# Kernel optimization log

Hardware: AMD Instinct MI355X
Metric: run time of the kernel (lower is better)

The kernel has to match this reference:

```python
import jax, jax.numpy as jnp
import numpy as np

B, S, D, H, R = 8, 1024, 1024, 8, 32
DH = D // H  # 128


def setup_inputs() -> dict:
    key = jax.random.key(0)
    ks = jax.random.split(key, 10)
    p = lambda k, shape: jax.random.normal(k, shape, dtype=jnp.float32) * 0.02
    return {
        "x": jax.random.normal(ks[0], (B, S, D), dtype=jnp.float32),
        "Uq": p(ks[1], (H, DH, R)), "Vq": p(ks[2], (H, R, DH)), "bq": p(ks[3], (H, DH)),
        "Uk": p(ks[4], (H, DH, R)), "Vk": p(ks[5], (H, R, DH)), "bk": p(ks[6], (H, DH)),
        "Uv": p(ks[7], (H, DH, R)), "Vv": p(ks[8], (H, R, DH)), "bv": p(ks[9], (H, DH)),
    }


def _lowrank(xh, U, V, b):
    # xh: [B,S,H,DH]; per-head factored linear y = x @ V^T @ U^T + b
    t = jnp.einsum('bshd,hrd->bshr', xh, V)          # down-project to rank R
    return jnp.einsum('bshr,hdr->bshd', t, U) + b    # up-project back to DH


def reference(x, Uq, Vq, bq, Uk, Vk, bk, Uv, Vv, bv):
    b_, s_, _ = x.shape
    xh = x.reshape(b_, s_, H, DH)                    # split heads (matches head-slice loop)
    q = _lowrank(xh, Uq, Vq, bq)
    k = _lowrank(xh, Uk, Vk, bk)
    v = _lowrank(xh, Uv, Vv, bv)
    scores = jnp.einsum('bqhd,bkhd->bhqk', q, k) / (DH ** 0.5)
    attn = jax.nn.softmax(scores, axis=-1)
    out = jnp.einsum('bhqk,bkhd->bqhd', attn, v)
    return out.reshape(b_, s_, D)                    # hstack over heads == reshape
```

## Files before the change

kernel.cpp:

```cpp
#include <hip/hip_runtime.h>
#include <cstdint>
#include <cstddef>

#define H 8
#define DH 128
#define RNK 32
#define SS 1024
#define BB 8
#define DD 1024

typedef __bf16 bf16x8 __attribute__((ext_vector_type(8)));
typedef float f32x4 __attribute__((ext_vector_type(4)));

#define QSCALE (1.4426950408889634f / 11.313708498984761f)

__device__ __forceinline__ unsigned short f2bf(float f) {
  unsigned int u = __builtin_bit_cast(unsigned int, f);
  return (unsigned short)((u + 0x7FFFu + ((u >> 16) & 1u)) >> 16);
}

__device__ __forceinline__ unsigned int cvtpk_bf16(float lo, float hi) {
  unsigned int r;
  asm("v_cvt_pk_bf16_f32 %0, %1, %2" : "=v"(r) : "v"(lo), "v"(hi));
  return r;
}

__device__ __forceinline__ void gload_lds16(const void* g, void* l) {
  __builtin_amdgcn_global_load_lds((const __attribute__((address_space(1))) void*)g,
                                   (__attribute__((address_space(3))) void*)l, 16, 0, 0);
}

__device__ __forceinline__ bf16x8 lds_frag(const unsigned short* base, int row, int kbyte,
                                           int rowbytes, int mask) {
  int off = row * rowbytes + kbyte;
  off ^= (row & mask) << 4;
  return *reinterpret_cast<const bf16x8*>(reinterpret_cast<const char*>(base) + off);
}

__global__ __launch_bounds__(256) void wcomb_kernel(
    const float* __restrict__ Uq, const float* __restrict__ Vq,
    const float* __restrict__ Uk, const float* __restrict__ Vk,
    const float* __restrict__ Uv, const float* __restrict__ Vv,
    unsigned short* __restrict__ Wc) {
  const int p = blockIdx.x / H, h = blockIdx.x % H;
  const int quarter = blockIdx.y;
  const float* U = (p == 0) ? Uq : ((p == 1) ? Uk : Uv);
  const float* V = (p == 0) ? Vq : ((p == 1) ? Vk : Vv);
  const float scale = (p == 0) ? QSCALE : 1.0f;
  U += (size_t)h * DH * RNK;
  V += (size_t)h * RNK * DH;
  __shared__ float Vl[RNK * DH];
  {
#pragma unroll
    for (int j = 0; j < 4; ++j) {
      const int f4 = threadIdx.x + j * 256;
      *reinterpret_cast<float4*>(&Vl[f4 * 4]) = *reinterpret_cast<const float4*>(V + f4 * 4);
    }
  }
  __syncthreads();
  const int dout = quarter * 32 + (threadIdx.x >> 3);
  const int c0 = (threadIdx.x & 7) * 16;
  float Ur[RNK];
#pragma unroll
  for (int j = 0; j < 8; ++j) {
    const float4 u4 = *reinterpret_cast<const float4*>(U + dout * RNK + j * 4);
    Ur[j * 4 + 0] = u4.x * scale; Ur[j * 4 + 1] = u4.y * scale;
    Ur[j * 4 + 2] = u4.z * scale; Ur[j * 4 + 3] = u4.w * scale;
  }
  float acc[16];
#pragma unroll
  for (int j = 0; j < 16; ++j) acc[j] = 0.f;
  for (int r = 0; r < RNK; ++r) {
    const float ur = Ur[r];
#pragma unroll
    for (int j = 0; j < 16; ++j) acc[j] += ur * Vl[r * DH + c0 + j];
  }
  unsigned short* outp = Wc + ((size_t)(p * H + h) * DH + dout) * DH + c0;
#pragma unroll
  for (int j4 = 0; j4 < 4; ++j4) {
    ushort4 o;
    o.x = f2bf(acc[j4 * 4 + 0]); o.y = f2bf(acc[j4 * 4 + 1]);
    o.z = f2bf(acc[j4 * 4 + 2]); o.w = f2bf(acc[j4 * 4 + 3]);
    *reinterpret_cast<ushort4*>(outp + j4 * 4) = o;
  }
}

__global__ __launch_bounds__(256, 4) void proj_kernel(
    const float* __restrict__ x, const unsigned short* __restrict__ Wc,
    const float* __restrict__ bq, const float* __restrict__ bk, const float* __restrict__ bv,
    unsigned short* __restrict__ Qp, unsigned short* __restrict__ Kp, unsigned short* __restrict__ Vt) {
  const int mt = blockIdx.x;
  const int h  = blockIdx.y;
  const int tid = threadIdx.x;
  const int wid = tid >> 6;
  const int lane = tid & 63;
  const int lr = lane & 15, lk = lane >> 4;

  __shared__ unsigned short xs[128 * 128];

  {
    const float* xb = x + (size_t)(mt * 128) * DD + h * DH;
    const int c4 = tid & 31, r0 = tid >> 5;
#pragma unroll
    for (int i = 0; i < 16; ++i) {
      const int r = r0 + i * 8;
      const float4 v = *reinterpret_cast<const float4*>(xb + (size_t)r * DD + c4 * 4);
      int off = r * 256 + c4 * 8; off ^= (r & 15) << 4;
      ushort4 o;
      o.x = f2bf(v.x); o.y = f2bf(v.y); o.z = f2bf(v.z); o.w = f2bf(v.w);
      *reinterpret_cast<ushort4*>(reinterpret_cast<char*>(xs) + off) = o;
    }
  }
  __syncthreads();

  for (int p = 0; p < 3; ++p) {
    const unsigned short* Wg = Wc + ((size_t)(p * H + h) << 14);
    f32x4 acc[2][8];
#pragma unroll
    for (int m = 0; m < 2; ++m)
#pragma unroll
      for (int n = 0; n < 8; ++n) acc[m][n] = {0.f, 0.f, 0.f, 0.f};

    if (p < 2) {
#pragma unroll
      for (int kk = 0; kk < 4; ++kk) {
        bf16x8 a[2], bfr[8];
#pragma unroll
        for (int m = 0; m < 2; ++m)
          a[m] = *reinterpret_cast<const bf16x8*>(Wg + (wid * 32 + m * 16 + lr) * 128 + kk * 32 + lk * 8);
#pragma unroll
        for (int n = 0; n < 8; ++n) bfr[n] = lds_frag(xs, n * 16 + lr, kk * 64 + lk * 16, 256, 15);
#pragma unroll
        for (int m = 0; m < 2; ++m)
#pragma unroll
          for (int n = 0; n < 8; ++n)
            acc[m][n] = __builtin_amdgcn_mfma_f32_16x16x32_bf16(a[m], bfr[n], acc[m][n], 0, 0, 0);
      }
      const float bs = (p == 0) ? QSCALE : 1.0f;
      const float* bias = ((p == 0) ? bq : bk) + h * DH;
      unsigned short* dst = ((p == 0) ? Qp : Kp);
#pragma unroll
      for (int m = 0; m < 2; ++m) {
        const int d0 = wid * 32 + m * 16 + lk * 4;
        const float4 bbv = *reinterpret_cast<const float4*>(bias + d0);
#pragma unroll
        for (int n = 0; n < 8; ++n) {
          const int tok = mt * 128 + n * 16 + lr;
          const int b = tok >> 10, si = tok & 1023;
          ushort4 o;
          o.x = f2bf(acc[m][n][0] + bbv.x * bs);
          o.y = f2bf(acc[m][n][1] + bbv.y * bs);
          o.z = f2bf(acc[m][n][2] + bbv.z * bs);
          o.w = f2bf(acc[m][n][3] + bbv.w * bs);
          *reinterpret_cast<ushort4*>(dst + ((size_t)(b * H + h) * SS + si) * DH + d0) = o;
        }
      }
    } else {
#pragma unroll
      for (int kk = 0; kk < 4; ++kk) {
        bf16x8 a[2], bfr[8];
#pragma unroll
        for (int m = 0; m < 2; ++m) a[m] = lds_frag(xs, wid * 32 + m * 16 + lr, kk * 64 + lk * 16, 256, 15);
#pragma unroll
        for (int n = 0; n < 8; ++n)
          bfr[n] = *reinterpret_cast<const bf16x8*>(Wg + (n * 16 + lr) * 128 + kk * 32 + lk * 8);
#pragma unroll
        for (int m = 0; m < 2; ++m)
#pragma unroll
          for (int n = 0; n < 8; ++n)
            acc[m][n] = __builtin_amdgcn_mfma_f32_16x16x32_bf16(a[m], bfr[n], acc[m][n], 0, 0, 0);
      }
      const float* bias = bv + h * DH;
#pragma unroll
      for (int n = 0; n < 8; ++n) {
        const int d = n * 16 + lr;
        const float bbs = bias[d];
#pragma unroll
        for (int m = 0; m < 2; ++m) {
          const int tok0 = mt * 128 + wid * 32 + m * 16 + lk * 4;
          const int b = tok0 >> 10, s0 = tok0 & 1023;
          ushort4 o;
          o.x = f2bf(acc[m][n][0] + bbs);
          o.y = f2bf(acc[m][n][1] + bbs);
          o.z = f2bf(acc[m][n][2] + bbs);
          o.w = f2bf(acc[m][n][3] + bbs);
          *reinterpret_cast<ushort4*>(Vt + ((size_t)(b * H + h) * DH + d) * SS + s0) = o;
        }
      }
    }
  }
}

__global__ __launch_bounds__(256, 2) void attn_kernel(
    const unsigned short* __restrict__ Qp, const unsigned short* __restrict__ Kp,
    const unsigned short* __restrict__ Vt, float* __restrict__ outp) {
  const int id = blockIdx.x;
  const int xcd = id & 7;
  const int bh = xcd * 8 + (id >> 6);
  const int qt = (id >> 3) & 7;
  const int b = bh >> 3, h = bh & 7;
  const int tid = threadIdx.x, wid = tid >> 6, lane = tid & 63;
  const int lr = lane & 15, lk = lane >> 4;

  __shared__ unsigned short ks[2][64 * 128];
  __shared__ unsigned short vs[2][128 * 64];

  const char* Kg = (const char*)(Kp + (size_t)bh * (SS * DH));
  const char* Vg = (const char*)(Vt + (size_t)bh * (DH * SS));

#define STAGE_K(KT, BUF)                                                            \
  {                                                                                 \
    _Pragma("unroll")                                                               \
    for (int c4 = 0; c4 < 4; ++c4) {                                                \
      const int c = wid * 4 + c4;                                                   \
      const int row = c * 4 + (lane >> 4);                                          \
      const int colb = ((lane & 15) << 4) ^ ((row & 15) << 4);                      \
      gload_lds16(Kg + (size_t)((KT) * 64 + row) * 256 + colb,                      \
                  (char*)(ks[BUF]) + c * 1024);                                     \
    }                                                                               \
  }
#define STAGE_V(KT, BUF)                                                            \
  {                                                                                 \
    _Pragma("unroll")                                                               \
    for (int c4 = 0; c4 < 4; ++c4) {                                                \
      const int c = wid * 4 + c4;                                                   \
      const int row = c * 8 + (lane >> 3);                                          \
      const int colb = ((lane & 7) << 4) ^ ((row & 7) << 4);                        \
      gload_lds16(Vg + (size_t)row * 2048 + (KT) * 128 + colb,                      \
                  (char*)(vs[BUF]) + c * 1024);                                     \
    }                                                                               \
  }

  STAGE_K(0, 0);
  STAGE_V(0, 0);

  bf16x8 qa[2][4];
  {
    const unsigned short* Qg = Qp + (size_t)bh * (SS * DH) + (size_t)(qt * 128 + wid * 32) * DH;
#pragma unroll
    for (int m = 0; m < 2; ++m)
#pragma unroll
      for (int kk = 0; kk < 4; ++kk)
        qa[m][kk] = *reinterpret_cast<const bf16x8*>(Qg + (m * 16 + lr) * DH + kk * 32 + lk * 8);
  }

  f32x4 oacc[2][8];
#pragma unroll
  for (int m = 0; m < 2; ++m)
#pragma unroll
    for (int n = 0; n < 8; ++n) oacc[m][n] = {0.f, 0.f, 0.f, 0.f};
  float lrow[2] = {0.f, 0.f};

  for (int kt = 0; kt < 16; ++kt) {
    __syncthreads();
    const int cur = kt & 1;
    if (kt < 15) {
      STAGE_K(kt + 1, cur ^ 1);
      STAGE_V(kt + 1, cur ^ 1);
    }
    const unsigned short* kb = ks[cur];
    const unsigned short* vb = vs[cur];

    f32x4 sacc[2][4];
#pragma unroll
    for (int m = 0; m < 2; ++m)
#pragma unroll
      for (int n = 0; n < 4; ++n) sacc[m][n] = {0.f, 0.f, 0.f, 0.f};
    __builtin_amdgcn_s_setprio(1);
#pragma unroll
    for (int kk = 0; kk < 4; ++kk) {
      bf16x8 kf[4];
#pragma unroll
      for (int n = 0; n < 4; ++n) kf[n] = lds_frag(kb, n * 16 + lr, kk * 64 + lk * 16, 256, 15);
#pragma unroll
      for (int n = 0; n < 4; ++n)
#pragma unroll
        for (int m = 0; m < 2; ++m)
          sacc[m][n] = __builtin_amdgcn_mfma_f32_16x16x32_bf16(kf[n], qa[m][kk], sacc[m][n], 0, 0, 0);
    }
    __builtin_amdgcn_s_setprio(0);

#pragma unroll
    for (int m = 0; m < 2; ++m) {
      float s = 0.f;
#pragma unroll
      for (int n = 0; n < 4; ++n)
#pragma unroll
        for (int r = 0; r < 4; ++r) {
          const float pv = exp2f(sacc[m][n][r]);
          sacc[m][n][r] = pv;
          s += pv;
        }
      lrow[m] += s;
    }

    bf16x8 pa[2][2];
#pragma unroll
    for (int m = 0; m < 2; ++m) {
      unsigned int pk0[4], pk1[4];
#pragma unroll
      for (int n = 0; n < 4; ++n) {
        pk0[n] = cvtpk_bf16(sacc[m][n][0], sacc[m][n][1]);
        pk1[n] = cvtpk_bf16(sacc[m][n][2], sacc[m][n][3]);
      }
#pragma unroll
      for (int kk2 = 0; kk2 < 2; ++kk2) {
        unsigned int w[4];
#pragma unroll
        for (int j = 0; j < 4; ++j) {
          const unsigned int lo = (j & 1) ? pk1[2 * kk2] : pk0[2 * kk2];
          const unsigned int hi = (j & 1) ? pk1[2 * kk2 + 1] : pk0[2 * kk2 + 1];
          const unsigned int sel = (lk & 2) ? hi : lo;
          const int srcl = lr + 16 * ((lk & 1) * 2 + (j >> 1));
          w[j] = (unsigned int)__shfl((int)sel, srcl);
        }
        uint4 t; t.x = w[0]; t.y = w[1]; t.z = w[2]; t.w = w[3];
        pa[m][kk2] = __builtin_bit_cast(bf16x8, t);
      }
    }

    __builtin_amdgcn_s_setprio(1);
#pragma unroll
    for (int kk2 = 0; kk2 < 2; ++kk2) {
#pragma unroll
      for (int n = 0; n < 8; ++n) {
        const bf16x8 vf = lds_frag(vb, n * 16 + lr, kk2 * 64 + lk * 16, 128, 7);
#pragma unroll
        for (int m = 0; m < 2; ++m)
          oacc[m][n] = __builtin_amdgcn_mfma_f32_16x16x32_bf16(pa[m][kk2], vf, oacc[m][n], 0, 0, 0);
      }
    }
    __builtin_amdgcn_s_setprio(0);
  }

#pragma unroll
  for (int m = 0; m < 2; ++m) {
    float red = lrow[m];
    red += __shfl_xor(red, 16);
    red += __shfl_xor(red, 32);
#pragma unroll
    for (int r = 0; r < 4; ++r) {
      const float lsum = __shfl(red, lk * 4 + r);
      const float inv = 1.f / lsum;
      const int srow = qt * 128 + wid * 32 + m * 16 + lk * 4 + r;
      float* og = outp + ((size_t)b * SS + srow) * DD + h * DH;
#pragma unroll
      for (int n = 0; n < 8; ++n) og[n * 16 + lr] = oacc[m][n][r] * inv;
    }
  }
}

extern "C" void kernel_launch(void* const* d_in, const int* in_sizes, int n_in,
                              void* d_out, int out_size, void* d_ws, size_t ws_size,
                              hipStream_t stream) {
  const float* x  = (const float*)d_in[0];
  const float* Uq = (const float*)d_in[1];
  const float* Vq = (const float*)d_in[2];
  const float* bq = (const float*)d_in[3];
  const float* Uk = (const float*)d_in[4];
  const float* Vk = (const float*)d_in[5];
  const float* bk = (const float*)d_in[6];
  const float* Uv = (const float*)d_in[7];
  const float* Vv = (const float*)d_in[8];
  const float* bv = (const float*)d_in[9];
  float* outp = (float*)d_out;

  unsigned short* Wc = (unsigned short*)d_ws;
  unsigned short* Qp = Wc + (size_t)3 * H * DH * DH;
  unsigned short* Kp = Qp + (size_t)BB * H * SS * DH;
  unsigned short* Vt = Kp + (size_t)BB * H * SS * DH;

  wcomb_kernel<<<dim3(24, 4), dim3(256), 0, stream>>>(Uq, Vq, Uk, Vk, Uv, Vv, Wc);
  proj_kernel<<<dim3(64, 8), dim3(256), 0, stream>>>(x, Wc, bq, bk, bv, Qp, Kp, Vt);
  attn_kernel<<<dim3(512), dim3(256), 0, stream>>>(Qp, Kp, Vt, outp);
}
```

Measured before the change: 199.5 us.

## Halve projection tile and stage Q/K/V outputs through LDS for coalesced stores

The projection kernel now processes 64-token tiles instead of 128, doubling the grid to 1024 blocks for better CU occupancy. Each projected Q, K and V tile is written to a swizzled shared-memory staging buffer and then copied to global memory with 16-byte coalesced stores, replacing the scattered 8-byte stores. This adds extra barriers and an LDS round-trip per projection, and each weight tile is reloaded by twice as many blocks.

```diff
diff --git a/kernel.cpp b/kernel.cpp
--- a/kernel.cpp
+++ b/kernel.cpp
@@ -95,14 +95,17 @@
   const int wid = tid >> 6;
   const int lane = tid & 63;
   const int lr = lane & 15, lk = lane >> 4;
-
-  __shared__ unsigned short xs[128 * 128];
+  const int bb_ = mt >> 4;
+  const int srow0 = (mt & 15) * 64;
+
+  __shared__ unsigned short xs[64 * 128];
+  __shared__ unsigned short ot[64 * 128];
 
   {
-    const float* xb = x + (size_t)(mt * 128) * DD + h * DH;
+    const float* xb = x + (size_t)(mt * 64) * DD + h * DH;
     const int c4 = tid & 31, r0 = tid >> 5;
 #pragma unroll
-    for (int i = 0; i < 16; ++i) {
+    for (int i = 0; i < 8; ++i) {
       const int r = r0 + i * 8;
       const float4 v = *reinterpret_cast<const float4*>(xb + (size_t)r * DD + c4 * 4);
       int off = r * 256 + c4 * 8; off ^= (r & 15) << 4;
@@ -115,77 +118,93 @@
 
   for (int p = 0; p < 3; ++p) {
     const unsigned short* Wg = Wc + ((size_t)(p * H + h) << 14);
-    f32x4 acc[2][8];
-#pragma unroll
-    for (int m = 0; m < 2; ++m)
-#pragma unroll
-      for (int n = 0; n < 8; ++n) acc[m][n] = {0.f, 0.f, 0.f, 0.f};
 
     if (p < 2) {
+      f32x4 acc[2][4];
+#pragma unroll
+      for (int m = 0; m < 2; ++m)
+#pragma unroll
+        for (int n = 0; n < 4; ++n) acc[m][n] = {0.f, 0.f, 0.f, 0.f};
 #pragma unroll
       for (int kk = 0; kk < 4; ++kk) {
-        bf16x8 a[2], bfr[8];
+        bf16x8 a[2], bfr[4];
 #pragma unroll
         for (int m = 0; m < 2; ++m)
           a[m] = *reinterpret_cast<const bf16x8*>(Wg + (wid * 32 + m * 16 + lr) * 128 + kk * 32 + lk * 8);
 #pragma unroll
-        for (int n = 0; n < 8; ++n) bfr[n] = lds_frag(xs, n * 16 + lr, kk * 64 + lk * 16, 256, 15);
+        for (int n = 0; n < 4; ++n) bfr[n] = lds_frag(xs, n * 16 + lr, kk * 64 + lk * 16, 256, 15);
 #pragma unroll
         for (int m = 0; m < 2; ++m)
 #pragma unroll
-          for (int n = 0; n < 8; ++n)
+          for (int n = 0; n < 4; ++n)
             acc[m][n] = __builtin_amdgcn_mfma_f32_16x16x32_bf16(a[m], bfr[n], acc[m][n], 0, 0, 0);
       }
       const float bs = (p == 0) ? QSCALE : 1.0f;
       const float* bias = ((p == 0) ? bq : bk) + h * DH;
-      unsigned short* dst = ((p == 0) ? Qp : Kp);
+      __syncthreads();
 #pragma unroll
       for (int m = 0; m < 2; ++m) {
         const int d0 = wid * 32 + m * 16 + lk * 4;
         const float4 bbv = *reinterpret_cast<const float4*>(bias + d0);
 #pragma unroll
-        for (int n = 0; n < 8; ++n) {
-          const int tok = mt * 128 + n * 16 + lr;
-          const int b = tok >> 10, si = tok & 1023;
+        for (int n = 0; n < 4; ++n) {
+          const int tok = n * 16 + lr;
+          int off = tok * 256 + d0 * 2; off ^= (tok & 7) << 4;
           ushort4 o;
           o.x = f2bf(acc[m][n][0] + bbv.x * bs);
           o.y = f2bf(acc[m][n][1] + bbv.y * bs);
           o.z = f2bf(acc[m][n][2] + bbv.z * bs);
           o.w = f2bf(acc[m][n][3] + bbv.w * bs);
-          *reinterpret_cast<ushort4*>(dst + ((size_t)(b * H + h) * SS + si) * DH + d0) = o;
+          *reinterpret_cast<ushort4*>(reinterpret_cast<char*>(ot) + off) = o;
         }
       }
+      __syncthreads();
+      unsigned short* dstb = ((p == 0) ? Qp : Kp) + ((size_t)(bb_ * H + h) * SS + srow0) * DH;
+#pragma unroll
+      for (int it = 0; it < 4; ++it) {
+        const int idx = tid + it * 256;
+        const int row = idx >> 4, chunk = idx & 15;
+        const int off = row * 256 + ((chunk * 16) ^ ((row & 7) << 4));
+        const uint4 v = *reinterpret_cast<const uint4*>(reinterpret_cast<const char*>(ot) + off);
+        *reinterpret_cast<uint4*>(dstb + (size_t)row * DH + chunk * 8) = v;
+      }
     } else {
+      f32x4 acc[8];
+#pragma unroll
+      for (int n = 0; n < 8; ++n) acc[n] = {0.f, 0.f, 0.f, 0.f};
 #pragma unroll
       for (int kk = 0; kk < 4; ++kk) {
-        bf16x8 a[2], bfr[8];
-#pragma unroll
-        for (int m = 0; m < 2; ++m) a[m] = lds_frag(xs, wid * 32 + m * 16 + lr, kk * 64 + lk * 16, 256, 15);
-#pragma unroll
-        for (int n = 0; n < 8; ++n)
-          bfr[n] = *reinterpret_cast<const bf16x8*>(Wg + (n * 16 + lr) * 128 + kk * 32 + lk * 8);
-#pragma unroll
-        for (int m = 0; m < 2; ++m)
-#pragma unroll
-          for (int n = 0; n < 8; ++n)
-            acc[m][n] = __builtin_amdgcn_mfma_f32_16x16x32_bf16(a[m], bfr[n], acc[m][n], 0, 0, 0);
+        const bf16x8 a = lds_frag(xs, wid * 16 + lr, kk * 64 + lk * 16, 256, 15);
+#pragma unroll
+        for (int n = 0; n < 8; ++n) {
+          const bf16x8 bfr = *reinterpret_cast<const bf16x8*>(Wg + (n * 16 + lr) * 128 + kk * 32 + lk * 8);
+          acc[n] = __builtin_amdgcn_mfma_f32_16x16x32_bf16(a, bfr, acc[n], 0, 0, 0);
+        }
       }
       const float* bias = bv + h * DH;
+      __syncthreads();
 #pragma unroll
       for (int n = 0; n < 8; ++n) {
         const int d = n * 16 + lr;
         const float bbs = bias[d];
-#pragma unroll
-        for (int m = 0; m < 2; ++m) {
-          const int tok0 = mt * 128 + wid * 32 + m * 16 + lk * 4;
-          const int b = tok0 >> 10, s0 = tok0 & 1023;
-          ushort4 o;
-          o.x = f2bf(acc[m][n][0] + bbs);
-          o.y = f2bf(acc[m][n][1] + bbs);
-          o.z = f2bf(acc[m][n][2] + bbs);
-          o.w = f2bf(acc[m][n][3] + bbs);
-          *reinterpret_cast<ushort4*>(Vt + ((size_t)(b * H + h) * DH + d) * SS + s0) = o;
-        }
+        const int tok0 = wid * 16 + lk * 4;
+        int off = d * 128 + tok0 * 2; off ^= (d & 7) << 4;
+        ushort4 o;
+        o.x = f2bf(acc[n][0] + bbs);
+        o.y = f2bf(acc[n][1] + bbs);
+        o.z = f2bf(acc[n][2] + bbs);
+        o.w = f2bf(acc[n][3] + bbs);
+        *reinterpret_cast<ushort4*>(reinterpret_cast<char*>(ot) + off) = o;
+      }
+      __syncthreads();
+      unsigned short* dstb = Vt + ((size_t)(bb_ * H + h) * DH) * SS + srow0;
+#pragma unroll
+      for (int it = 0; it < 4; ++it) {
+        const int idx = tid + it * 256;
+        const int row = idx >> 3, chunk = idx & 7;
+        const int off = row * 128 + ((chunk * 16) ^ ((row & 7) << 4));
+        const uint4 v = *reinterpret_cast<const uint4*>(reinterpret_cast<const char*>(ot) + off);
+        *reinterpret_cast<uint4*>(dstb + (size_t)row * SS + chunk * 8) = v;
       }
     }
   }
@@ -371,6 +390,6 @@
   unsigned short* Vt = Kp + (size_t)BB * H * SS * DH;
 
   wcomb_kernel<<<dim3(24, 4), dim3(256), 0, stream>>>(Uq, Vq, Uk, Vk, Uv, Vv, Wc);
-  proj_kernel<<<dim3(64, 8), dim3(256), 0, stream>>>(x, Wc, bq, bk, bv, Qp, Kp, Vt);
+  proj_kernel<<<dim3(128, 8), dim3(256), 0, stream>>>(x, Wc, bq, bk, bv, Qp, Kp, Vt);
   attn_kernel<<<dim3(512), dim3(256), 0, stream>>>(Qp, Kp, Vt, outp);
 }
```

Result: faster. 171.9 us (-13.9%).
